# Kernel tuning notes

Measured on AMD Instinct MI355X. Metric: run time of the kernel, lower is better.

## Reference

```python
import jax, jax.numpy as jnp
import numpy as np

N, D = 8192, 128
WEIGHT = 0.01


def _neg_flat_indices(n):
    # Replicates: mask = ones(n,n); fill_diagonal_(0); mask[i,i+1]=0; mask[i+1,i]=0
    # i.e. keep (i,j) with j != i, j != i+1, j != i-1. Row-major flatnonzero
    # reproduces torch's sim[mask] flattening order exactly.
    i = np.arange(n)[:, None]
    j = np.arange(n)[None, :]
    mask = (j != i) & (j != i + 1) & (j != i - 1)
    idx = np.flatnonzero(mask)
    assert idx.size == (n - 1) * (n - 2)
    return idx


NEG_IDX = jnp.asarray(_neg_flat_indices(N))  # [(N-1)*(N-2)] int32/int64 constant


def setup_inputs() -> dict:
    key = jax.random.key(0)
    factor = jax.random.normal(key, (N, D), dtype=jnp.float32)
    return {"factor": factor}


def reference(factor):
    n = factor.shape[0]
    # F.normalize(factor): L2-normalize rows with eps=1e-12
    norms = jnp.linalg.norm(factor, axis=1, keepdims=True)
    f = factor / jnp.maximum(norms, 1e-12)
    sim = f @ f.T                                   # [N, N] gram matrix
    pos = jnp.diagonal(sim, offset=1).reshape(n - 1, 1)      # [N-1, 1]
    neg = sim.reshape(-1)[NEG_IDX].reshape(n - 1, n - 2)     # [N-1, N-2]
    logits = jnp.concatenate([pos, neg], axis=1)             # [N-1, N-1]
    # CrossEntropyLoss(reduction='sum') with all-zero labels:
    # sum_i (logsumexp(logits_i) - logits_i[0])
    loss = jnp.sum(jax.nn.logsumexp(logits, axis=1) - logits[:, 0])
    loss = loss / n
    return -WEIGHT * loss
```

## Files before the change

### kernel.cpp

```cpp
#include <hip/hip_runtime.h>
#include <hip/hip_bf16.h>
#include <hip/hip_fp8.h>

#define N 8192
#define D 128
#define WEIGHT 0.01f
#define NTILES 64
#define NBLK 2080

typedef float floatx4 __attribute__((ext_vector_type(4)));

__global__ __launch_bounds__(256) void k_norm(const float* __restrict__ x,
                                              unsigned char* __restrict__ fb8,
                                              float* __restrict__ out) {
    int gid = blockIdx.x * 256 + threadIdx.x;
    if (gid == 0) out[0] = 0.0f;
    int row = gid >> 4;
    int c   = gid & 15;
    const float4* xr = (const float4*)(x + (size_t)row * D + c * 8);
    float4 f0 = xr[0], f1 = xr[1];
    float s = f0.x * f0.x + f0.y * f0.y + f0.z * f0.z + f0.w * f0.w
            + f1.x * f1.x + f1.y * f1.y + f1.z * f1.z + f1.w * f1.w;
    s += __shfl_xor(s, 1, 64);
    s += __shfl_xor(s, 2, 64);
    s += __shfl_xor(s, 4, 64);
    s += __shfl_xor(s, 8, 64);
    float inv = 1.0f / fmaxf(sqrtf(s), 1e-12f);
    union { unsigned char b[8]; uint2 u; } pk;
    pk.b[0] = __hip_fp8_e4m3(f0.x * inv).__x;
    pk.b[1] = __hip_fp8_e4m3(f0.y * inv).__x;
    pk.b[2] = __hip_fp8_e4m3(f0.z * inv).__x;
    pk.b[3] = __hip_fp8_e4m3(f0.w * inv).__x;
    pk.b[4] = __hip_fp8_e4m3(f1.x * inv).__x;
    pk.b[5] = __hip_fp8_e4m3(f1.y * inv).__x;
    pk.b[6] = __hip_fp8_e4m3(f1.z * inv).__x;
    pk.b[7] = __hip_fp8_e4m3(f1.w * inv).__x;
    int cc = c >> 1, h = c & 1;
    ((uint2*)fb8)[(size_t)row * 16 + (((cc ^ (row & 7)) << 1) | h)] = pk.u;
}

__global__ __launch_bounds__(256, 4) void k_gram(const unsigned char* __restrict__ fb8,
                                                 float* __restrict__ Prow,
                                                 float* __restrict__ Pcol,
                                                 float* __restrict__ p,
                                                 float* __restrict__ ep) {
    int b = blockIdx.x;
    int bi = (int)((2.0 * NTILES + 1.0 - sqrt((2.0 * NTILES + 1.0) * (2.0 * NTILES + 1.0) - 8.0 * (double)b)) * 0.5);
    while (bi * NTILES - bi * (bi - 1) / 2 > b) --bi;
    while ((bi + 1) * NTILES - (bi + 1) * bi / 2 <= b) ++bi;
    int bj = bi + (b - (bi * NTILES - bi * (bi - 1) / 2));

    __shared__ uint4 Ab[1024];
    __shared__ uint4 Bb[1024];
    __shared__ float PR[2][128];
    __shared__ float PC[2][128];

    const int t = threadIdx.x;
    const int lane = t & 63;
    const int wid  = t >> 6;
    const int wrow = wid >> 1, wcol = wid & 1;
    const int col0 = lane & 15;
    const int quad = lane >> 4;
    const int rbase = bi * 128, cbase = bj * 128;

    const uint4* gA = (const uint4*)fb8 + (size_t)rbase * 8;
    const uint4* gB = (const uint4*)fb8 + (size_t)cbase * 8;
    #pragma unroll
    for (int i = 0; i < 4; ++i) {
        int ca = wid * 256 + i * 64;
        __builtin_amdgcn_global_load_lds(
            (const __attribute__((address_space(1))) void*)(gA + ca + lane),
            (__attribute__((address_space(3))) void*)&Ab[ca], 16, 0, 0);
        __builtin_amdgcn_global_load_lds(
            (const __attribute__((address_space(1))) void*)(gB + ca + lane),
            (__attribute__((address_space(3))) void*)&Bb[ca], 16, 0, 0);
    }
    __syncthreads();

    floatx4 acc[4][4];
    #pragma unroll
    for (int a = 0; a < 4; ++a)
        #pragma unroll
        for (int c = 0; c < 4; ++c)
            acc[a][c] = (floatx4){0.0f, 0.0f, 0.0f, 0.0f};

    const long* A8 = (const long*)Ab;
    const long* B8 = (const long*)Bb;
    const int swz = (col0 & 7);
    #pragma unroll
    for (int ks = 0; ks < 4; ++ks) {
        long af[4], bfr[4];
        int cc = ks * 2 + (quad >> 1);
        int off = quad & 1;
        int base8 = ((cc ^ swz) << 1) | off;
        #pragma unroll
        for (int mt = 0; mt < 4; ++mt) {
            int rl = wrow * 64 + mt * 16 + col0;
            af[mt] = A8[rl * 16 + base8];
        }
        #pragma unroll
        for (int nt = 0; nt < 4; ++nt) {
            int cl = wcol * 64 + nt * 16 + col0;
            bfr[nt] = B8[cl * 16 + base8];
        }
        #pragma unroll
        for (int mt = 0; mt < 4; ++mt)
            #pragma unroll
            for (int nt = 0; nt < 4; ++nt)
                acc[mt][nt] = __builtin_amdgcn_mfma_f32_16x16x32_fp8_fp8(af[mt], bfr[nt], acc[mt][nt], 0, 0, 0);
    }

    float v[16];
    float colpart[4];
    #pragma unroll
    for (int m = 0; m < 16; ++m) v[m] = 0.0f;
    #pragma unroll
    for (int m = 0; m < 4; ++m) colpart[m] = 0.0f;

    if (bj > bi + 1) {
        #pragma unroll
        for (int mt = 0; mt < 4; ++mt)
            #pragma unroll
            for (int nt = 0; nt < 4; ++nt)
                #pragma unroll
                for (int reg = 0; reg < 4; ++reg) {
                    float e = __expf(acc[mt][nt][reg]);
                    v[mt * 4 + reg] += e;
                    colpart[nt] += e;
                }
    } else {
        #pragma unroll
        for (int mt = 0; mt < 4; ++mt)
            #pragma unroll
            for (int nt = 0; nt < 4; ++nt)
                #pragma unroll
                for (int reg = 0; reg < 4; ++reg) {
                    int r = rbase + wrow * 64 + mt * 16 + quad * 4 + reg;
                    int c = cbase + wcol * 64 + nt * 16 + col0;
                    float s0 = acc[mt][nt][reg];
                    float e = __expf(s0);
                    if (c == r + 1) { p[r] = s0; ep[r] = e; }
                    e = (c > r) ? e : 0.0f;
                    v[mt * 4 + reg] += e;
                    colpart[nt] += e;
                }
    }

    float v8[8];
    #pragma unroll
    for (int k = 0; k < 8; ++k) {
        float a = v[2 * k], bb = v[2 * k + 1];
        float give = (lane & 1) ? a : bb;
        float keep = (lane & 1) ? bb : a;
        v8[k] = keep + __shfl_xor(give, 1, 64);
    }
    float v4[4];
    #pragma unroll
    for (int k = 0; k < 4; ++k) {
        float a = v8[2 * k], bb = v8[2 * k + 1];
        float give = (lane & 2) ? a : bb;
        float keep = (lane & 2) ? bb : a;
        v4[k] = keep + __shfl_xor(give, 2, 64);
    }
    float v2[2];
    #pragma unroll
    for (int k = 0; k < 2; ++k) {
        float a = v4[2 * k], bb = v4[2 * k + 1];
        float give = (lane & 4) ? a : bb;
        float keep = (lane & 4) ? bb : a;
        v2[k] = keep + __shfl_xor(give, 4, 64);
    }
    {
        float a = v2[0], bb = v2[1];
        float give = (lane & 8) ? a : bb;
        float keep = (lane & 8) ? bb : a;
        float v1 = keep + __shfl_xor(give, 8, 64);
        int rowl = wrow * 64 + (col0 >> 2) * 16 + quad * 4 + (col0 & 3);
        PR[wcol][rowl] = v1;
    }
    {
        float c2[2];
        #pragma unroll
        for (int k = 0; k < 2; ++k) {
            float a = colpart[2 * k];
            float bb = colpart[2 * k + 1];
            float give = (lane & 16) ? a : bb;
            float keep = (lane & 16) ? bb : a;
            c2[k] = keep + __shfl_xor(give, 16, 64);
        }
        float a = c2[0], bb = c2[1];
        float give = (lane & 32) ? a : bb;
        float keep = (lane & 32) ? bb : a;
        float cv = keep + __shfl_xor(give, 32, 64);
        PC[wrow][wcol * 64 + lane] = cv;
    }
    __syncthreads();

    if (t < 128) {
        Prow[(size_t)b * 128 + t] = PR[0][t] + PR[1][t];
    } else {
        int c = t - 128;
        Pcol[(size_t)b * 128 + c] = PC[0][c] + PC[1][c];
    }
}

__global__ __launch_bounds__(256) void k_tail(const float* __restrict__ Prow,
                                              const float* __restrict__ Pcol,
                                              const float* __restrict__ p,
                                              const float* __restrict__ ep,
                                              float* __restrict__ out) {
    __shared__ float Ush[128];
    __shared__ float Lsh[128];
    __shared__ float sw[4];
    int band = blockIdx.x;
    int t = threadIdx.x;
    if (t < 128) {
        int baseU = band * NTILES - band * (band - 1) / 2;
        float s = 0.0f;
        for (int bj = band; bj < NTILES; ++bj)
            s += Prow[(size_t)(baseU + bj - band) * 128 + t];
        Ush[t] = s;
    } else {
        int c = band * 128 + (t - 128) + 1;
        float s = 0.0f;
        if (c < N) {
            int bc = c >> 7;
            for (int bi = 0; bi <= bc; ++bi)
                s += Pcol[(size_t)(bi * NTILES - bi * (bi - 1) / 2 + (bc - bi)) * 128 + (c & 127)];
        }
        Lsh[t - 128] = s;
    }
    __syncthreads();
    float term = 0.0f;
    if (t < 128) {
        int r = band * 128 + t;
        if (r < N - 1)
            term = __logf(Ush[t] + Lsh[t] - ep[r]) - p[r];
    }
    #pragma unroll
    for (int m = 1; m < 64; m <<= 1) term += __shfl_xor(term, m, 64);
    int lane = t & 63, wd = t >> 6;
    if (lane == 0) sw[wd] = term;
    __syncthreads();
    if (t == 0) {
        float part = sw[0] + sw[1] + sw[2] + sw[3];
        atomicAdd(out, -WEIGHT * part / (float)N);
    }
}

extern "C" void kernel_launch(void* const* d_in, const int* in_sizes, int n_in,
                              void* d_out, int out_size, void* d_ws, size_t ws_size,
                              hipStream_t stream) {
    const float* x = (const float*)d_in[0];
    float* out = (float*)d_out;
    char* ws = (char*)d_ws;
    unsigned char* fb8 = (unsigned char*)ws;
    float* p    = (float*)(ws + (size_t)N * D);
    float* ep   = p + N;
    float* Prow = ep + N;
    float* Pcol = Prow + (size_t)NBLK * 128;

    hipLaunchKernelGGL(k_norm, dim3(512),  dim3(256), 0, stream, x, fb8, out);
    hipLaunchKernelGGL(k_gram, dim3(NBLK), dim3(256), 0, stream, fb8, Prow, Pcol, p, ep);
    hipLaunchKernelGGL(k_tail, dim3(64),   dim3(256), 0, stream, Prow, Pcol, p, ep, out);
}
```

Before: 91.59 us.

## Fold log2e into fp8 scale, use exp2, recompute positive logit in tail

Normalized rows are scaled by sqrt(log2 e) before fp8 quantization, so the gram accumulator holds log2e-scaled similarities and the epilogue can use exp2f instead of expf. The per-element diagonal bookkeeping that wrote p/ep from k_gram is removed. Only diagonal tiles now take the masked path. The tail recomputes each positive logit as an fp8 dot product of adjacent rows and converts back with LN2. This cuts scattered stores and branch work in the gram epilogue, at the cost of a small extra dot-product loop in the tail.

```diff
diff --git a/kernel.cpp b/kernel.cpp
--- a/kernel.cpp
+++ b/kernel.cpp
@@ -7,8 +7,14 @@
 #define WEIGHT 0.01f
 #define NTILES 64
 #define NBLK 2080
+#define KSCALE 1.2011224087864498f
+#define LN2 0.6931471805599453f
 
 typedef float floatx4 __attribute__((ext_vector_type(4)));
+
+__device__ __forceinline__ float fp8_to_f32(unsigned char b) {
+    __hip_fp8_e4m3 v; v.__x = b; return (float)v;
+}
 
 __global__ __launch_bounds__(256) void k_norm(const float* __restrict__ x,
                                               unsigned char* __restrict__ fb8,
@@ -25,7 +31,7 @@
     s += __shfl_xor(s, 2, 64);
     s += __shfl_xor(s, 4, 64);
     s += __shfl_xor(s, 8, 64);
-    float inv = 1.0f / fmaxf(sqrtf(s), 1e-12f);
+    float inv = KSCALE / fmaxf(sqrtf(s), 1e-12f);
     union { unsigned char b[8]; uint2 u; } pk;
     pk.b[0] = __hip_fp8_e4m3(f0.x * inv).__x;
     pk.b[1] = __hip_fp8_e4m3(f0.y * inv).__x;
@@ -41,9 +47,7 @@
 
 __global__ __launch_bounds__(256, 4) void k_gram(const unsigned char* __restrict__ fb8,
                                                  float* __restrict__ Prow,
-                                                 float* __restrict__ Pcol,
-                                                 float* __restrict__ p,
-                                                 float* __restrict__ ep) {
+                                                 float* __restrict__ Pcol) {
     int b = blockIdx.x;
     int bi = (int)((2.0 * NTILES + 1.0 - sqrt((2.0 * NTILES + 1.0) * (2.0 * NTILES + 1.0) - 8.0 * (double)b)) * 0.5);
     while (bi * NTILES - bi * (bi - 1) / 2 > b) --bi;
@@ -117,14 +121,14 @@
     #pragma unroll
     for (int m = 0; m < 4; ++m) colpart[m] = 0.0f;
 
-    if (bj > bi + 1) {
+    if (bj > bi) {
         #pragma unroll
         for (int mt = 0; mt < 4; ++mt)
             #pragma unroll
             for (int nt = 0; nt < 4; ++nt)
                 #pragma unroll
                 for (int reg = 0; reg < 4; ++reg) {
-                    float e = __expf(acc[mt][nt][reg]);
+                    float e = exp2f(acc[mt][nt][reg]);
                     v[mt * 4 + reg] += e;
                     colpart[nt] += e;
                 }
@@ -135,12 +139,10 @@
             for (int nt = 0; nt < 4; ++nt)
                 #pragma unroll
                 for (int reg = 0; reg < 4; ++reg) {
-                    int r = rbase + wrow * 64 + mt * 16 + quad * 4 + reg;
-                    int c = cbase + wcol * 64 + nt * 16 + col0;
-                    float s0 = acc[mt][nt][reg];
-                    float e = __expf(s0);
-                    if (c == r + 1) { p[r] = s0; ep[r] = e; }
-                    e = (c > r) ? e : 0.0f;
+                    int rl = wrow * 64 + mt * 16 + quad * 4 + reg;
+                    int cl = wcol * 64 + nt * 16 + col0;
+                    float e = exp2f(acc[mt][nt][reg]);
+                    e = (cl > rl) ? e : 0.0f;
                     v[mt * 4 + reg] += e;
                     colpart[nt] += e;
                 }
@@ -204,22 +206,36 @@
     }
 }
 
-__global__ __launch_bounds__(256) void k_tail(const float* __restrict__ Prow,
+__global__ __launch_bounds__(256) void k_tail(const unsigned char* __restrict__ fb8,
+                                              const float* __restrict__ Prow,
                                               const float* __restrict__ Pcol,
-                                              const float* __restrict__ p,
-                                              const float* __restrict__ ep,
                                               float* __restrict__ out) {
-    __shared__ float Ush[128];
     __shared__ float Lsh[128];
     __shared__ float sw[4];
     int band = blockIdx.x;
     int t = threadIdx.x;
+    float Ureg = 0.0f, pp = 0.0f;
     if (t < 128) {
+        int r = band * 128 + t;
+        if (r < N - 1) {
+            const uint4* g = (const uint4*)fb8;
+            float s = 0.0f;
+            #pragma unroll
+            for (int cc = 0; cc < 8; ++cc) {
+                union { uint4 u; unsigned char b[16]; } ua, ub;
+                ua.u = g[(size_t)r * 8 + (cc ^ (r & 7))];
+                ub.u = g[(size_t)(r + 1) * 8 + (cc ^ ((r + 1) & 7))];
+                #pragma unroll
+                for (int k = 0; k < 16; ++k)
+                    s += fp8_to_f32(ua.b[k]) * fp8_to_f32(ub.b[k]);
+            }
+            pp = s;
+        }
         int baseU = band * NTILES - band * (band - 1) / 2;
         float s = 0.0f;
         for (int bj = band; bj < NTILES; ++bj)
             s += Prow[(size_t)(baseU + bj - band) * 128 + t];
-        Ush[t] = s;
+        Ureg = s;
     } else {
         int c = band * 128 + (t - 128) + 1;
         float s = 0.0f;
@@ -235,7 +251,7 @@
     if (t < 128) {
         int r = band * 128 + t;
         if (r < N - 1)
-            term = __logf(Ush[t] + Lsh[t] - ep[r]) - p[r];
+            term = __logf(Ureg + Lsh[t] - exp2f(pp)) - LN2 * pp;
     }
     #pragma unroll
     for (int m = 1; m < 64; m <<= 1) term += __shfl_xor(term, m, 64);
@@ -255,12 +271,10 @@
     float* out = (float*)d_out;
     char* ws = (char*)d_ws;
     unsigned char* fb8 = (unsigned char*)ws;
-    float* p    = (float*)(ws + (size_t)N * D);
-    float* ep   = p + N;
-    float* Prow = ep + N;
+    float* Prow = (float*)(ws + (size_t)N * D);
     float* Pcol = Prow + (size_t)NBLK * 128;
 
     hipLaunchKernelGGL(k_norm, dim3(512),  dim3(256), 0, stream, x, fb8, out);
-    hipLaunchKernelGGL(k_gram, dim3(NBLK), dim3(256), 0, stream, fb8, Prow, Pcol, p, ep);
-    hipLaunchKernelGGL(k_tail, dim3(64),   dim3(256), 0, stream, Prow, Pcol, p, ep, out);
-}
+    hipLaunchKernelGGL(k_gram, dim3(NBLK), dim3(256), 0, stream, fb8, Prow, Pcol);
+    hipLaunchKernelGGL(k_tail, dim3(64),   dim3(256), 0, stream, fb8, Prow, Pcol, out);
+}
```

Result: no change. 92.89 us (+1.4%).
